# Kernel tuning notes

Hardware: AMD Instinct MI355X
Metric: run time of the kernel (lower is better)

## Reference

```python
import jax, jax.numpy as jnp
import numpy as np

HEADS = 12
HEAD_DIM = 64          # dim_out // heads = 768 // 12
Q_STRIDE = 4
WINDOW_SIZE = 16       # post-pool tokens per window; pre-pool = Q_STRIDE*WINDOW_SIZE = 64
DIM = 768
DIM_OUT = 768


def setup_inputs() -> dict:
    key = jax.random.key(0)
    k1, k2, k3 = jax.random.split(key, 3)
    B, N = 32, 3136
    x = jax.random.normal(k1, (B, N, DIM), dtype=jnp.float32)
    Wqkv = jax.random.normal(k2, (DIM, 3 * DIM_OUT), dtype=jnp.float32) * 0.02
    bqkv = jnp.zeros((3 * DIM_OUT,), dtype=jnp.float32)
    Wproj = jax.random.normal(k3, (DIM_OUT, DIM_OUT), dtype=jnp.float32) * 0.02
    bproj = jnp.zeros((DIM_OUT,), dtype=jnp.float32)
    return {"x": x, "Wqkv": Wqkv, "bqkv": bqkv, "Wproj": Wproj, "bproj": bproj}


def reference(x, Wqkv, bqkv, Wproj, bproj):
    B, N, _ = x.shape
    num_windows = N // (Q_STRIDE * WINDOW_SIZE)  # 49
    scale = HEAD_DIM ** (-0.5)

    # QKV projection (torch Linear uses x @ W^T; here Wqkv is stored [dim, 3*dim_out])
    qkv = x @ Wqkv + bqkv                                  # [B, N, 3*dim_out]
    # Same reshape as torch: windows are the inner split of the token axis
    qkv = qkv.reshape(B, N // num_windows, num_windows, 3, HEADS, HEAD_DIM)
    qkv = jnp.transpose(qkv, (3, 0, 4, 2, 1, 5))           # [3, B, h, w, t, d]
    q, k, v = qkv[0], qkv[1], qkv[2]                       # t = Q_STRIDE*WINDOW_SIZE

    # Query max-pooling over stride groups
    q = q.reshape(B, HEADS, num_windows, Q_STRIDE, WINDOW_SIZE, HEAD_DIM).max(axis=3)
    # q: [B, h, w, WINDOW_SIZE, d]

    # Scaled dot-product attention within each window
    logits = jnp.einsum('bhwqd,bhwkd->bhwqk', q, k) * scale
    attn = jax.nn.softmax(logits, axis=-1)
    o = jnp.einsum('bhwqk,bhwkd->bhwqd', attn, v)          # [B, h, w, q, d]

    # transpose(1,3) then flatten tokens, channels = heads*head_dim
    o = jnp.transpose(o, (0, 3, 2, 1, 4)).reshape(B, -1, DIM_OUT)
    return o @ Wproj + bproj
```

## Files before the change

### kernel.cpp

```cpp
#include <hip/hip_runtime.h>
#include <hip/hip_bf16.h>


typedef __bf16 bf16x8 __attribute__((ext_vector_type(8)));
typedef float f32x4 __attribute__((ext_vector_type(4)));
typedef unsigned short u16x8 __attribute__((ext_vector_type(8)));

#define GLOBAL_AS __attribute__((address_space(1)))
#define LDS_AS __attribute__((address_space(3)))

__device__ __forceinline__ unsigned short f2bf(float f) {
    unsigned u = __builtin_bit_cast(unsigned, f);
    u += 0x7FFFu + ((u >> 16) & 1u);
    return (unsigned short)(u >> 16);
}
__device__ __forceinline__ float bf2f(unsigned short h) {
    return __builtin_bit_cast(float, (unsigned)h << 16);
}

__device__ __forceinline__ void load16_to_lds(const void* g, void* l) {
    __builtin_amdgcn_global_load_lds((const GLOBAL_AS unsigned int*)g,
                                     (LDS_AS unsigned int*)l, 16, 0, 0);
}

__global__ void cvt_permute(const float* __restrict__ in,
                            unsigned short* __restrict__ out, int nRows) {
    const long idx = (long)blockIdx.x * blockDim.x + threadIdx.x;
    if (idx >= (long)nRows * 192) return;
    const int g  = (int)(idx / 192);
    const int c4 = (int)(idx - (long)g * 192);
    const int b  = g / 3136;
    const int nn = g - b * 3136;
    const int t  = nn / 49;
    const int w  = nn - t * 49;
    float4 f = ((const float4*)in)[idx];
    uint2 u;
    u.x = (unsigned)f2bf(f.x) | ((unsigned)f2bf(f.y) << 16);
    u.y = (unsigned)f2bf(f.z) | ((unsigned)f2bf(f.w) << 16);
    ((uint2*)out)[(long)(b * 3136 + w * 64 + t) * 192 + c4] = u;
}

__global__ void transpose_cvt(const float* __restrict__ W,
                              unsigned short* __restrict__ Wt, int K, int N) {
    __shared__ float tile[32][33];
    int bx = blockIdx.x * 32;
    int by = blockIdx.y * 32;
    int tx = threadIdx.x & 31, ty = threadIdx.x >> 5;
    #pragma unroll
    for (int i = 0; i < 32; i += 8)
        tile[ty + i][tx] = W[(size_t)(by + ty + i) * N + bx + tx];
    __syncthreads();
    #pragma unroll
    for (int i = 0; i < 32; i += 8)
        Wt[(size_t)(bx + ty + i) * K + by + tx] = f2bf(tile[tx][ty + i]);
}

#define VM_WAIT2 asm volatile("s_waitcnt vmcnt(2)" ::: "memory")
#define VM_WAIT0 asm volatile("s_waitcnt vmcnt(0)" ::: "memory")

#define GPHASE(BUF, CSW, IH, LOADBG, STG, WAITS) do {                        \
    if (LOADBG) {                                                            \
        const unsigned short* bb = &ls[(BUF) * 32768 + 16384 + (CSW)];       \
        bg[0] = *(const bf16x8*)&bb[(wn +  0 + lane15) * 64];                \
        bg[1] = *(const bf16x8*)&bb[(wn + 16 + lane15) * 64];                \
        bg[2] = *(const bf16x8*)&bb[(wn + 32 + lane15) * 64];                \
        bg[3] = *(const bf16x8*)&bb[(wn + 48 + lane15) * 64];                \
    }                                                                        \
    {                                                                        \
        const unsigned short* ab = &ls[(BUF) * 32768 + (CSW)];               \
        af[0] = *(const bf16x8*)&ab[(wm + (IH)*64 +  0 + lane15) * 64];      \
        af[1] = *(const bf16x8*)&ab[(wm + (IH)*64 + 16 + lane15) * 64];      \
        af[2] = *(const bf16x8*)&ab[(wm + (IH)*64 + 32 + lane15) * 64];      \
        af[3] = *(const bf16x8*)&ab[(wm + (IH)*64 + 48 + lane15) * 64];      \
    }                                                                        \
    STG;                                                                     \
    WAITS;                                                                   \
    __builtin_amdgcn_s_barrier();                                            \
    asm volatile("s_waitcnt lgkmcnt(0)" ::: "memory");                       \
    __builtin_amdgcn_sched_barrier(0);                                       \
    __builtin_amdgcn_s_setprio(1);                                           \
    _Pragma("unroll")                                                        \
    for (int ii = 0; ii < 4; ++ii)                                           \
        _Pragma("unroll")                                                    \
        for (int j = 0; j < 4; ++j)                                          \
            acc[(IH)*4 + ii][j] = __builtin_amdgcn_mfma_f32_16x16x32_bf16(   \
                bg[j], af[ii], acc[(IH)*4 + ii][j], 0, 0, 0);                \
    __builtin_amdgcn_s_setprio(0);                                           \
    __builtin_amdgcn_s_barrier();                                            \
} while (0)

template <bool OUT_BF16>
__global__ __launch_bounds__(512, 2)
void gemm_bt256(const unsigned short* __restrict__ A,
                const unsigned short* __restrict__ Bt,
                const float* __restrict__ bias,
                void* __restrict__ Cv, int mBase, int N, int K) {
    __shared__ alignas(16) unsigned short ls[65536];

    const int tid  = threadIdx.x;
    const int lane = tid & 63;
    const int wave = tid >> 6;
    const int wm = (wave >> 2) * 128;
    const int wn = (wave & 3) * 64;
    const int lane15 = lane & 15;
    const int quad   = lane >> 4;
    const int csw0 = ((quad    ) ^ (lane & 7)) * 8;
    const int csw1 = ((quad + 4) ^ (lane & 7)) * 8;

    const int nwg = (int)(gridDim.x * gridDim.y);
    const int hid = (int)(blockIdx.y * gridDim.x + blockIdx.x);
    const int q8  = nwg >> 3, r8 = nwg & 7;
    const int xcd = hid & 7;
    const int lid = (xcd < r8 ? xcd * (q8 + 1) : r8 * (q8 + 1) + (xcd - r8) * q8)
                    + (hid >> 3);
    const int tileX = lid % (int)gridDim.x;
    const int tileY = lid / (int)gridDim.x;
    const long bm = (long)tileY * 256;
    const long bn = (long)tileX * 256;

    const int r0 = tid >> 3;
    const int lc = (tid & 7) ^ (r0 & 7);
    const unsigned short* gA = A  + (bm + r0) * (long)K + lc * 8;
    const unsigned short* gB = Bt + (bn + r0) * (long)K + lc * 8;
    const int ldsWaveBase = wave * 512;

    auto STAGE_A = [&](int buf, int q, int kt) {
        load16_to_lds(gA + (long)q * 64 * K + kt * 64,
                      &ls[buf * 32768 + q * 4096 + ldsWaveBase]);
    };
    auto STAGE_B = [&](int buf, int q, int kt) {
        load16_to_lds(gB + (long)q * 64 * K + kt * 64,
                      &ls[buf * 32768 + 16384 + q * 4096 + ldsWaveBase]);
    };

    f32x4 acc[8][4] = {};
    bf16x8 af[4], bg[4];

    const int NT = K >> 6;
    const int NI = NT >> 1;

    STAGE_A(0, 0, 0); STAGE_A(0, 1, 0); STAGE_A(0, 2, 0); STAGE_A(0, 3, 0);
    STAGE_B(0, 0, 0); STAGE_B(0, 1, 0); STAGE_B(0, 2, 0); STAGE_B(0, 3, 0);
    STAGE_A(1, 0, 1); STAGE_A(1, 2, 1);
    VM_WAIT2;
    __builtin_amdgcn_s_barrier();

    for (int i = 0; i < NI; ++i) {
        const int t2 = 2 * i;
        const bool last = (i == NI - 1);
        GPHASE(0, csw0, 0, 1,
               { STAGE_A(1, 1, t2 + 1); STAGE_A(1, 3, t2 + 1); STAGE_B(1, 0, t2 + 1); },
               { (void)0; });
        GPHASE(0, csw0, 1, 0,
               { STAGE_B(1, 1, t2 + 1); STAGE_B(1, 2, t2 + 1); STAGE_B(1, 3, t2 + 1); },
               { (void)0; });
        GPHASE(0, csw1, 0, 1, { (void)0; }, { (void)0; });
        GPHASE(0, csw1, 1, 0,
               { if (!last) { STAGE_A(0, 0, t2 + 2); STAGE_A(0, 2, t2 + 2); } },
               { if (last) { VM_WAIT0; } else { VM_WAIT2; } });
        GPHASE(1, csw0, 0, 1,
               { if (!last) { STAGE_A(0, 1, t2 + 2); STAGE_A(0, 3, t2 + 2); } },
               { (void)0; });
        GPHASE(1, csw0, 1, 0,
               { if (!last) { STAGE_B(0, 0, t2 + 2); STAGE_B(0, 1, t2 + 2); } },
               { (void)0; });
        GPHASE(1, csw1, 0, 1,
               { if (!last) { STAGE_B(0, 2, t2 + 2); STAGE_B(0, 3, t2 + 2); } },
               { (void)0; });
        GPHASE(1, csw1, 1, 0,
               { if (!last) { STAGE_A(1, 0, t2 + 3); STAGE_A(1, 2, t2 + 3); VM_WAIT2; } },
               { (void)0; });
    }

    const int rbase = (int)(bm) + wm + lane15;
    if constexpr (OUT_BF16) {
        const int colBase = (int)bn + wn;
        const int sec = colBase / 768;
        const int hh  = (colBase - sec * 768) >> 6;
        const long shOff = (long)sec * 49152 + hh * 4096 + quad * 4;
        unsigned short* qout = (unsigned short*)Cv;
        float4 bv[4];
        #pragma unroll
        for (int j = 0; j < 4; ++j)
            bv[j] = *(const float4*)&bias[colBase + quad * 4 + j * 16];
        #pragma unroll
        for (int i = 0; i < 8; ++i) {
            const int m  = mBase + rbase + i * 16;
            const int b  = m / 3136;
            const int r3 = m - b * 3136;
            unsigned short* rp = qout + (long)(b * 49 + (r3 >> 6)) * 147456
                                      + shOff + (long)(r3 & 63) * 64;
            #pragma unroll
            for (int j = 0; j < 4; ++j) {
                ushort4 s;
                s.x = f2bf(acc[i][j][0] + bv[j].x);
                s.y = f2bf(acc[i][j][1] + bv[j].y);
                s.z = f2bf(acc[i][j][2] + bv[j].z);
                s.w = f2bf(acc[i][j][3] + bv[j].w);
                *(ushort4*)(rp + j * 16) = s;
            }
        }
    } else {
        const int cbase = (int)bn + wn + quad * 4;
        #pragma unroll
        for (int j = 0; j < 4; ++j) {
            const int col = cbase + j * 16;
            const float4 bv = *(const float4*)&bias[col];
            #pragma unroll
            for (int i = 0; i < 8; ++i) {
                const long row = (long)mBase + rbase + i * 16;
                const size_t idx = (size_t)row * N + col;
                float4 s;
                s.x = acc[i][j][0] + bv.x;
                s.y = acc[i][j][1] + bv.y;
                s.z = acc[i][j][2] + bv.z;
                s.w = acc[i][j][3] + bv.w;
                *(float4*)((float*)Cv + idx) = s;
            }
        }
    }
}

__global__ __launch_bounds__(256)
void attn_win_mfma(const unsigned short* __restrict__ qkv,
                   unsigned short* __restrict__ o) {
    const int hg = blockIdx.x;
    const int w  = blockIdx.y;
    const int b  = blockIdx.z;
    const int wave = threadIdx.x >> 6;
    const int lane = threadIdx.x & 63;
    const int h = hg * 4 + wave;
    const int l = lane & 15;
    const int quad = lane >> 4;

    __shared__ alignas(16) unsigned short vT[4][64 * 72];
    __shared__ alignas(16) unsigned short ps[4][16 * 72];

    const long slab = (long)(b * 49 + w) * 147456;
    const long hOff = (long)h * 4096;

    bf16x8 af[2];
    {
        const unsigned short* qr = qkv + slab + hOff + (long)l * 64 + quad * 8;
        float m0[8], m1[8];
        #pragma unroll
        for (int sg = 0; sg < 4; ++sg) {
            uint4 u0 = *(const uint4*)(qr + sg * 1024);
            uint4 u1 = *(const uint4*)(qr + sg * 1024 + 32);
            const unsigned short* p0 = (const unsigned short*)&u0;
            const unsigned short* p1 = (const unsigned short*)&u1;
            #pragma unroll
            for (int e = 0; e < 8; ++e) {
                float f0 = bf2f(p0[e]), f1 = bf2f(p1[e]);
                if (sg == 0) { m0[e] = f0; m1[e] = f1; }
                else { m0[e] = fmaxf(m0[e], f0); m1[e] = fmaxf(m1[e], f1); }
            }
        }
        u16x8 a0, a1;
        #pragma unroll
        for (int e = 0; e < 8; ++e) {
            a0[e] = f2bf(m0[e] * 0.125f);
            a1[e] = f2bf(m1[e] * 0.125f);
        }
        af[0] = __builtin_bit_cast(bf16x8, a0);
        af[1] = __builtin_bit_cast(bf16x8, a1);
    }

    {
        const unsigned short* vr = qkv + slab + 98304 + hOff + (long)lane * 64;
        unsigned short* vw = &vT[wave][0];
        #pragma unroll
        for (int i = 0; i < 8; ++i) {
            uint4 u = *(const uint4*)(vr + i * 8);
            const unsigned short* pe = (const unsigned short*)&u;
            #pragma unroll
            for (int e = 0; e < 8; ++e)
                vw[(i * 8 + e) * 72 + lane] = pe[e];
        }
    }

    f32x4 Sc[4] = {};
    {
        bf16x8 bk0, bk1;
        #pragma unroll
        for (int tt = 0; tt < 4; ++tt) {
            const unsigned short* kr =
                qkv + slab + 49152 + hOff + (long)(tt * 16 + l) * 64 + quad * 8;
            bk0 = __builtin_bit_cast(bf16x8, *(const uint4*)kr);
            bk1 = __builtin_bit_cast(bf16x8, *(const uint4*)(kr + 32));
            Sc[tt] = __builtin_amdgcn_mfma_f32_16x16x32_bf16(af[0], bk0, Sc[tt], 0, 0, 0);
            Sc[tt] = __builtin_amdgcn_mfma_f32_16x16x32_bf16(af[1], bk1, Sc[tt], 0, 0, 0);
        }
    }

    float pr[4][4];
    {
        #pragma unroll
        for (int r = 0; r < 4; ++r) {
            float mx = fmaxf(fmaxf(Sc[0][r], Sc[1][r]), fmaxf(Sc[2][r], Sc[3][r]));
            #pragma unroll
            for (int off = 1; off < 16; off <<= 1)
                mx = fmaxf(mx, __shfl_xor(mx, off));
            float sum = 0.f;
            #pragma unroll
            for (int tt = 0; tt < 4; ++tt) {
                pr[tt][r] = __expf(Sc[tt][r] - mx);
                sum += pr[tt][r];
            }
            #pragma unroll
            for (int off = 1; off < 16; off <<= 1)
                sum += __shfl_xor(sum, off);
            const float inv = 1.0f / sum;
            #pragma unroll
            for (int tt = 0; tt < 4; ++tt) pr[tt][r] *= inv;
        }
    }

    {
        unsigned short* pw = &ps[wave][0];
        #pragma unroll
        for (int r = 0; r < 4; ++r)
            #pragma unroll
            for (int tt = 0; tt < 4; ++tt)
                pw[(quad * 4 + r) * 72 + tt * 16 + l] = f2bf(pr[tt][r]);
    }

    f32x4 Oc[4] = {};
    {
        #pragma unroll
        for (int s = 0; s < 2; ++s) {
            bf16x8 ap = *(const bf16x8*)&ps[wave][l * 72 + s * 32 + quad * 8];
            #pragma unroll
            for (int tt = 0; tt < 4; ++tt) {
                bf16x8 bv = *(const bf16x8*)&vT[wave][(tt * 16 + l) * 72 + s * 32 + quad * 8];
                Oc[tt] = __builtin_amdgcn_mfma_f32_16x16x32_bf16(ap, bv, Oc[tt], 0, 0, 0);
            }
        }
    }

    {
        const long obase = ((long)b * 784 + (long)(quad * 4) * 49 + w) * 768 + h * 64 + l;
        #pragma unroll
        for (int tt = 0; tt < 4; ++tt)
            #pragma unroll
            for (int r = 0; r < 4; ++r)
                o[obase + (long)r * 49 * 768 + tt * 16] = f2bf(Oc[tt][r]);
    }
}

extern "C" void kernel_launch(void* const* d_in, const int* in_sizes, int n_in,
                              void* d_out, int out_size, void* d_ws, size_t ws_size,
                              hipStream_t stream) {
    const float* x     = (const float*)d_in[0];
    const float* Wqkv  = (const float*)d_in[1];
    const float* bqkv  = (const float*)d_in[2];
    const float* Wproj = (const float*)d_in[3];
    const float* bproj = (const float*)d_in[4];
    float* out = (float*)d_out;

    const long needed1 = (32L * 3136 * 768 + 32L * 3136 * 2304 +
                          25088L * 768 + 2304L * 768 + 768L * 768) * 2;
    const int C  = (ws_size >= (size_t)needed1) ? 1 : 4;
    const int CB = 32 / C;
    const long XC = (long)CB * 3136 * 768;
    const long QC = (long)CB * 3136 * 2304;

    char* p = (char*)d_ws;
    unsigned short* xb    = (unsigned short*)p; p += XC * 2;
    unsigned short* qkvb  = (unsigned short*)p; p += QC * 2;
    unsigned short* ob    = (unsigned short*)p; p += 25088L * 768 * 2;
    unsigned short* WqkvT = (unsigned short*)p; p += 2304L * 768 * 2;
    unsigned short* WprojT= (unsigned short*)p; p += 768L * 768 * 2;

    transpose_cvt<<<dim3(72, 24), 256, 0, stream>>>(Wqkv, WqkvT, 768, 2304);
    transpose_cvt<<<dim3(24, 24), 256, 0, stream>>>(Wproj, WprojT, 768, 768);

    const int M  = CB * 3136;
    const int Mh = M / 2;
    for (int c = 0; c < C; ++c) {
        const int nRows = M;
        cvt_permute<<<(int)(((long)nRows * 192 + 255) / 256), 256, 0, stream>>>(
            x + (size_t)c * XC, xb, nRows);
        gemm_bt256<true><<<dim3(9, Mh / 256), 512, 0, stream>>>(
            xb, WqkvT, bqkv, qkvb, 0, 2304, 768);
        gemm_bt256<true><<<dim3(9, Mh / 256), 512, 0, stream>>>(
            xb + (long)Mh * 768, WqkvT, bqkv, qkvb, Mh, 2304, 768);
        attn_win_mfma<<<dim3(3, 49, CB), 256, 0, stream>>>(
            qkvb, ob + (size_t)c * CB * 784 * 768);
    }
    gemm_bt256<false><<<dim3(3, 98), 512, 0, stream>>>(
        ob, WprojT, bproj, out, 0, 768, 768);
}
```

Before: 1.068 ms.

## Widen cvt stores, merge weight transposes, swizzle attention LDS, split QKV GEMM

```diff
diff --git a/kernel.cpp b/kernel.cpp
--- a/kernel.cpp
+++ b/kernel.cpp
@@ -23,27 +23,38 @@
                                      (LDS_AS unsigned int*)l, 16, 0, 0);
 }
 
-__global__ void cvt_permute(const float* __restrict__ in,
-                            unsigned short* __restrict__ out, int nRows) {
-    const long idx = (long)blockIdx.x * blockDim.x + threadIdx.x;
-    if (idx >= (long)nRows * 192) return;
-    const int g  = (int)(idx / 192);
-    const int c4 = (int)(idx - (long)g * 192);
+__global__ __launch_bounds__(256)
+void cvt_permute(const float* __restrict__ in,
+                 unsigned short* __restrict__ out, int nRows) {
+    const int u = blockIdx.x * blockDim.x + threadIdx.x;
+    if (u >= nRows * 96) return;
+    const int g = u / 96;
+    const int c = u - g * 96;
     const int b  = g / 3136;
     const int nn = g - b * 3136;
     const int t  = nn / 49;
     const int w  = nn - t * 49;
-    float4 f = ((const float4*)in)[idx];
-    uint2 u;
-    u.x = (unsigned)f2bf(f.x) | ((unsigned)f2bf(f.y) << 16);
-    u.y = (unsigned)f2bf(f.z) | ((unsigned)f2bf(f.w) << 16);
-    ((uint2*)out)[(long)(b * 3136 + w * 64 + t) * 192 + c4] = u;
-}
-
-__global__ void transpose_cvt(const float* __restrict__ W,
-                              unsigned short* __restrict__ Wt, int K, int N) {
+    float4 f0 = ((const float4*)in)[(long)g * 192 + c * 2];
+    float4 f1 = ((const float4*)in)[(long)g * 192 + c * 2 + 1];
+    uint4 o;
+    o.x = (unsigned)f2bf(f0.x) | ((unsigned)f2bf(f0.y) << 16);
+    o.y = (unsigned)f2bf(f0.z) | ((unsigned)f2bf(f0.w) << 16);
+    o.z = (unsigned)f2bf(f1.x) | ((unsigned)f2bf(f1.y) << 16);
+    o.w = (unsigned)f2bf(f1.z) | ((unsigned)f2bf(f1.w) << 16);
+    ((uint4*)out)[(long)(b * 3136 + w * 64 + t) * 96 + c] = o;
+}
+
+__global__ void transpose_cvt2(const float* __restrict__ W0,
+                               unsigned short* __restrict__ T0,
+                               const float* __restrict__ W1,
+                               unsigned short* __restrict__ T1) {
     __shared__ float tile[32][33];
-    int bx = blockIdx.x * 32;
+    int bxi = blockIdx.x;
+    const float* W; unsigned short* Wt; int N;
+    if (bxi < 72) { W = W0; Wt = T0; N = 2304; }
+    else          { W = W1; Wt = T1; N = 768; bxi -= 72; }
+    const int K = 768;
+    int bx = bxi * 32;
     int by = blockIdx.y * 32;
     int tx = threadIdx.x & 31, ty = threadIdx.x >> 5;
     #pragma unroll
@@ -221,7 +232,7 @@
     }
 }
 
-__global__ __launch_bounds__(256)
+__global__ __launch_bounds__(256, 4)
 void attn_win_mfma(const unsigned short* __restrict__ qkv,
                    unsigned short* __restrict__ o) {
     const int hg = blockIdx.x;
@@ -233,8 +244,8 @@
     const int l = lane & 15;
     const int quad = lane >> 4;
 
-    __shared__ alignas(16) unsigned short vT[4][64 * 72];
-    __shared__ alignas(16) unsigned short ps[4][16 * 72];
+    __shared__ alignas(16) unsigned short vT[4][64 * 64];
+    __shared__ alignas(16) unsigned short ps[4][16 * 64];
 
     const long slab = (long)(b * 49 + w) * 147456;
     const long hOff = (long)h * 4096;
@@ -269,19 +280,23 @@
     {
         const unsigned short* vr = qkv + slab + 98304 + hOff + (long)lane * 64;
         unsigned short* vw = &vT[wave][0];
+        const int ch = lane >> 3, le = lane & 7;
         #pragma unroll
         for (int i = 0; i < 8; ++i) {
             uint4 u = *(const uint4*)(vr + i * 8);
             const unsigned short* pe = (const unsigned short*)&u;
             #pragma unroll
-            for (int e = 0; e < 8; ++e)
-                vw[(i * 8 + e) * 72 + lane] = pe[e];
+            for (int e = 0; e < 8; ++e) {
+                const int d = i * 8 + e;
+                vw[d * 64 + ((ch ^ (d & 7)) << 3) + le] = pe[e];
+            }
         }
     }
 
     f32x4 Sc[4] = {};
     {
         bf16x8 bk0, bk1;
+        __builtin_amdgcn_s_setprio(1);
         #pragma unroll
         for (int tt = 0; tt < 4; ++tt) {
             const unsigned short* kr =
@@ -291,6 +306,7 @@
             Sc[tt] = __builtin_amdgcn_mfma_f32_16x16x32_bf16(af[0], bk0, Sc[tt], 0, 0, 0);
             Sc[tt] = __builtin_amdgcn_mfma_f32_16x16x32_bf16(af[1], bk1, Sc[tt], 0, 0, 0);
         }
+        __builtin_amdgcn_s_setprio(0);
     }
 
     float pr[4][4];
@@ -319,23 +335,30 @@
     {
         unsigned short* pw = &ps[wave][0];
         #pragma unroll
-        for (int r = 0; r < 4; ++r)
-            #pragma unroll
-            for (int tt = 0; tt < 4; ++tt)
-                pw[(quad * 4 + r) * 72 + tt * 16 + l] = f2bf(pr[tt][r]);
+        for (int r = 0; r < 4; ++r) {
+            const int row = quad * 4 + r;
+            #pragma unroll
+            for (int tt = 0; tt < 4; ++tt) {
+                const int c = (tt << 1) + (l >> 3);
+                pw[row * 64 + ((c ^ (row & 7)) << 3) + (l & 7)] = f2bf(pr[tt][r]);
+            }
+        }
     }
 
     f32x4 Oc[4] = {};
     {
+        __builtin_amdgcn_s_setprio(1);
         #pragma unroll
         for (int s = 0; s < 2; ++s) {
-            bf16x8 ap = *(const bf16x8*)&ps[wave][l * 72 + s * 32 + quad * 8];
+            const int csw = (((s << 2) + quad) ^ (l & 7)) << 3;
+            bf16x8 ap = *(const bf16x8*)&ps[wave][l * 64 + csw];
             #pragma unroll
             for (int tt = 0; tt < 4; ++tt) {
-                bf16x8 bv = *(const bf16x8*)&vT[wave][(tt * 16 + l) * 72 + s * 32 + quad * 8];
+                bf16x8 bv = *(const bf16x8*)&vT[wave][(tt * 16 + l) * 64 + csw];
                 Oc[tt] = __builtin_amdgcn_mfma_f32_16x16x32_bf16(ap, bv, Oc[tt], 0, 0, 0);
             }
         }
+        __builtin_amdgcn_s_setprio(0);
     }
 
     {
@@ -372,19 +395,24 @@
     unsigned short* WqkvT = (unsigned short*)p; p += 2304L * 768 * 2;
     unsigned short* WprojT= (unsigned short*)p; p += 768L * 768 * 2;
 
-    transpose_cvt<<<dim3(72, 24), 256, 0, stream>>>(Wqkv, WqkvT, 768, 2304);
-    transpose_cvt<<<dim3(24, 24), 256, 0, stream>>>(Wproj, WprojT, 768, 768);
-
-    const int M  = CB * 3136;
-    const int Mh = M / 2;
+    transpose_cvt2<<<dim3(96, 24), 256, 0, stream>>>(Wqkv, WqkvT, Wproj, WprojT);
+
+    const int M = CB * 3136;
+    const int tiles = M / 256;
+    const int tc0 = (tiles + 2) / 3;
+    const int tc1 = (tiles - tc0 + 1) / 2;
+    const int tc2 = tiles - tc0 - tc1;
     for (int c = 0; c < C; ++c) {
-        const int nRows = M;
-        cvt_permute<<<(int)(((long)nRows * 192 + 255) / 256), 256, 0, stream>>>(
-            x + (size_t)c * XC, xb, nRows);
-        gemm_bt256<true><<<dim3(9, Mh / 256), 512, 0, stream>>>(
-            xb, WqkvT, bqkv, qkvb, 0, 2304, 768);
-        gemm_bt256<true><<<dim3(9, Mh / 256), 512, 0, stream>>>(
-            xb + (long)Mh * 768, WqkvT, bqkv, qkvb, Mh, 2304, 768);
+        cvt_permute<<<(M * 96 + 255) / 256, 256, 0, stream>>>(
+            x + (size_t)c * XC, xb, M);
+        int mb = 0;
+        const int tcs[3] = {tc0, tc1, tc2};
+        for (int s = 0; s < 3; ++s) {
+            if (tcs[s] > 0)
+                gemm_bt256<true><<<dim3(9, tcs[s]), 512, 0, stream>>>(
+                    xb + (long)mb * 768, WqkvT, bqkv, qkvb, mb, 2304, 768);
+            mb += tcs[s] * 256;
+        }
         attn_win_mfma<<<dim3(3, 49, CB), 256, 0, stream>>>(
             qkvb, ob + (size_t)c * CB * 784 * 768);
     }
```

Result: slower. 1.105 ms (+3.5%).
